# Kernel optimization log

Hardware: AMD Instinct MI355X
Metric: run time of the kernel (lower is better)

## Reference

```python
import jax, jax.numpy as jnp
import numpy as np

CHUNK = 64  # _HYMBA_SCAN_CHUNK default
HEAD_DIM = 128
STATE_DIM = 128


def setup_inputs() -> dict:
    key = jax.random.key(0)
    ks = jax.random.split(key, 6)
    B, T = 8, 8192
    x = jax.random.normal(ks[0], (B, T, HEAD_DIM), dtype=jnp.float32)
    log_A = jax.random.normal(ks[1], (STATE_DIM,), dtype=jnp.float32) * 0.5
    # torch Linear weights are (out_features, in_features); kaiming-uniform-ish init
    lim = 1.0 / np.sqrt(HEAD_DIM)
    W_B = jax.random.uniform(ks[2], (STATE_DIM, HEAD_DIM), jnp.float32, -lim, lim)
    W_C = jax.random.uniform(ks[3], (STATE_DIM, HEAD_DIM), jnp.float32, -lim, lim)
    W_dt = jax.random.uniform(ks[4], (STATE_DIM, HEAD_DIM), jnp.float32, -lim, lim)
    b_dt = jnp.full((STATE_DIM,), -4.0, dtype=jnp.float32)
    lim_o = 1.0 / np.sqrt(STATE_DIM)
    W_out = jax.random.uniform(ks[5], (HEAD_DIM, STATE_DIM), jnp.float32, -lim_o, lim_o)
    return {"x": x, "log_A": log_A, "W_B": W_B, "W_C": W_C,
            "W_dt": W_dt, "b_dt": b_dt, "W_out": W_out}


def _scan_chunks(log_a, u, chunk_size=CHUNK):
    # log_a, u: (B, T, S) fp32; exact chunk-parallel diagonal recurrence
    B, T, S = u.shape
    nc = T // chunk_size
    la = log_a.reshape(B, nc, chunk_size, S).transpose(1, 0, 2, 3)  # (nc,B,ck,S)
    uu = u.reshape(B, nc, chunk_size, S).transpose(1, 0, 2, 3)

    def step(h0, inp):
        la_c, u_c = inp                                   # (B, ck, S)
        log_p = jnp.clip(jnp.cumsum(la_c, axis=1), -30.0, 0.0)
        p = jnp.exp(log_p)
        h = p * jnp.cumsum(u_c * jnp.exp(-log_p), axis=1) + p * h0[:, None, :]
        return h[:, -1, :], h

    h0 = jnp.zeros((B, S), dtype=jnp.float32)
    _, h_chunks = jax.lax.scan(step, h0, (la, uu))        # (nc, B, ck, S)
    return h_chunks.transpose(1, 0, 2, 3).reshape(B, T, S)


def reference(x, log_A, W_B, W_C, W_dt, b_dt, W_out):
    xf = x.astype(jnp.float32)
    dt = jnp.minimum(jax.nn.softplus(jnp.einsum('btd,sd->bts', xf, W_dt) + b_dt), 1.0)
    A = -jnp.minimum(jnp.exp(log_A.astype(jnp.float32)), 10.0)   # (S,)
    log_a = jnp.clip(dt * A[None, None, :], -0.5, 0.0)
    Bx = jnp.einsum('btd,sd->bts', xf, W_B) * dt
    C = jnp.einsum('btd,sd->bts', xf, W_C)
    h = _scan_chunks(log_a, Bx)                                   # (B,T,S)
    y = jnp.sum(C * h, axis=-1, keepdims=True)                    # (B,T,1)
    out = jnp.einsum('bts,ds->btd', h.astype(x.dtype), W_out)
    return out + y.astype(x.dtype) * x[..., :1]
```

## Files before the change

### kernel.cpp

```cpp
#include <hip/hip_runtime.h>
#include <hip/hip_bf16.h>

#define B_ 8
#define T_ 8192
#define D_ 128
#define S_ 128
#define CK 64
#define NC 128
#define NCHUNK (B_*NC)
#define XSTR 140

typedef __attribute__((ext_vector_type(8))) __bf16 bf16x8;
typedef __attribute__((ext_vector_type(4))) float floatx4;

#define WS_WBF     0
#define WS_AVEC    32768
#define WS_PART    32896
#define WS_PARTI   (32896 + 262144)

__device__ __forceinline__ unsigned short f2bf(float f) {
  __hip_bfloat16 b = __float2bfloat16(f);
  return *(unsigned short*)&b;
}

__device__ __forceinline__ float softplus1(float z) {
  float sp = fmaxf(z, 0.0f) + __logf(1.0f + __expf(-fabsf(z)));
  return fminf(sp, 1.0f);
}

__device__ __forceinline__ unsigned long long part_load(const unsigned long long* p) {
  return __hip_atomic_load(p, __ATOMIC_RELAXED, __HIP_MEMORY_SCOPE_AGENT);
}
__device__ __forceinline__ void part_store(unsigned long long* p, unsigned long long v) {
  __hip_atomic_store(p, v, __ATOMIC_RELAXED, __HIP_MEMORY_SCOPE_AGENT);
}

__global__ __launch_bounds__(256) void k0_prep(
    const float* __restrict__ Wdt, const float* __restrict__ WB,
    const float* __restrict__ WC,  const float* __restrict__ Wout,
    const float* __restrict__ logA, float* __restrict__ ws) {
  unsigned short* wb = (unsigned short*)(ws + WS_WBF);
  const float* srcs[4] = {Wdt, WB, WC, Wout};
  int gid = blockIdx.x * 256 + threadIdx.x;
  if (gid < 8192) {
    int fid = gid;
    int lane = fid & 63;
    int kk   = (fid >> 6) & 3;
    int nt   = (fid >> 8) & 7;
    int m    = fid >> 11;
    int c = lane & 15, g = lane >> 4;
    const float* src = srcs[m] + (16 * nt + c) * 128 + 32 * kk + 8 * g;
    float4 v0 = *(const float4*)src;
    float4 v1 = *(const float4*)(src + 4);
    unsigned short o[8];
    o[0] = f2bf(v0.x); o[1] = f2bf(v0.y); o[2] = f2bf(v0.z); o[3] = f2bf(v0.w);
    o[4] = f2bf(v1.x); o[5] = f2bf(v1.y); o[6] = f2bf(v1.z); o[7] = f2bf(v1.w);
    *(ushort4*)&wb[fid * 8]     = *(ushort4*)&o[0];
    *(ushort4*)&wb[fid * 8 + 4] = *(ushort4*)&o[4];
  }
  unsigned long long* part = (unsigned long long*)(ws + WS_PART);
#pragma unroll
  for (int i = 0; i < 16; ++i)
    part[gid + 16384 * i] = 0ull;
  if (blockIdx.x == 0 && threadIdx.x < 128)
    ws[WS_AVEC + threadIdx.x] = -fminf(expf(logA[threadIdx.x]), 10.0f);
}

#define WFRAG(mat, nt, kk) \
  (*(const bf16x8*)&wb[(((((mat) * 8 + (nt)) * 4) + (kk)) * 64 + lane) * 8])

__global__ __launch_bounds__(256, 3) void k_main(
    const float* __restrict__ x, const float* __restrict__ bdt,
    float* __restrict__ out, float* __restrict__ ws) {
  __shared__ __align__(16) unsigned short xb[64 * XSTR];
  __shared__ float x0s[64];
  __shared__ float yxa[4 * 64];

  const int tid  = threadIdx.x;
  const int bc   = blockIdx.x;
  const int b    = bc & 7;
  const int cidx = bc >> 3;
  const long chunk_t0 = (long)b * T_ + (long)cidx * CK;
  const int w    = tid >> 6;
  const int lane = tid & 63;
  const int g    = lane >> 4;
  const int c    = lane & 15;

  float Av2[2], Bd2[2];
#pragma unroll
  for (int ntl = 0; ntl < 2; ++ntl) {
    int s = 32 * w + 16 * ntl + c;
    Av2[ntl] = ws[WS_AVEC + s];
    Bd2[ntl] = bdt[s];
  }

  const float4* x4 = (const float4*)(x + chunk_t0 * D_);
#pragma unroll
  for (int i = 0; i < 8; ++i) {
    int f4 = tid + 256 * i;
    int t  = f4 >> 5;
    int d0 = (f4 & 31) << 2;
    float4 v = x4[f4];
    ushort4 o;
    o.x = f2bf(v.x); o.y = f2bf(v.y); o.z = f2bf(v.z); o.w = f2bf(v.w);
    *(ushort4*)&xb[t * XSTR + d0] = o;
  }
  if (tid < 64) x0s[tid] = x[(chunk_t0 + tid) * D_];
  __syncthreads();

  const unsigned short* wb = (const unsigned short*)(ws + WS_WBF);
  unsigned long long* partA = (unsigned long long*)(ws + WS_PART);
  unsigned long long* partI = (unsigned long long*)(ws + WS_PARTI);

  floatx4 A_[2][4], U_[2][4];
#pragma unroll
  for (int ntl = 0; ntl < 2; ++ntl)
#pragma unroll
    for (int mt = 0; mt < 4; ++mt) {
      A_[ntl][mt] = (floatx4){0.f, 0.f, 0.f, 0.f};
      U_[ntl][mt] = (floatx4){0.f, 0.f, 0.f, 0.f};
    }
#pragma unroll
  for (int kk = 0; kk < 4; ++kk) {
    bf16x8 fD0 = WFRAG(0, 2 * w + 0, kk);
    bf16x8 fD1 = WFRAG(0, 2 * w + 1, kk);
    bf16x8 fB0 = WFRAG(1, 2 * w + 0, kk);
    bf16x8 fB1 = WFRAG(1, 2 * w + 1, kk);
#pragma unroll
    for (int mt = 0; mt < 4; ++mt) {
      bf16x8 a = *(const bf16x8*)&xb[(16 * mt + c) * XSTR + 8 * g + 32 * kk];
      A_[0][mt] = __builtin_amdgcn_mfma_f32_16x16x32_bf16(a, fD0, A_[0][mt], 0, 0, 0);
      A_[1][mt] = __builtin_amdgcn_mfma_f32_16x16x32_bf16(a, fD1, A_[1][mt], 0, 0, 0);
      U_[0][mt] = __builtin_amdgcn_mfma_f32_16x16x32_bf16(a, fB0, U_[0][mt], 0, 0, 0);
      U_[1][mt] = __builtin_amdgcn_mfma_f32_16x16x32_bf16(a, fB1, U_[1][mt], 0, 0, 0);
    }
  }

#pragma unroll
  for (int ntl = 0; ntl < 2; ++ntl)
#pragma unroll
    for (int mt = 0; mt < 4; ++mt)
#pragma unroll
      for (int i = 0; i < 4; ++i) {
        float dt = softplus1(A_[ntl][mt][i] + Bd2[ntl]);
        float u  = U_[ntl][mt][i] * dt;
        float la = fmaxf(fminf(dt * Av2[ntl], 0.0f), -0.5f);
        A_[ntl][mt][i] = __expf(la);
        U_[ntl][mt][i] = u;
      }

  float PcT[2], HcT[2];
#pragma unroll
  for (int ntl = 0; ntl < 2; ++ntl) {
    float Pc = 1.0f, Hc = 0.0f;
#pragma unroll
    for (int mt = 0; mt < 4; ++mt) {
      float P = A_[ntl][mt][0], H = U_[ntl][mt][0];
#pragma unroll
      for (int i = 1; i < 4; ++i) {
        H = fmaf(H, A_[ntl][mt][i], U_[ntl][mt][i]);
        P = P * A_[ntl][mt][i];
        A_[ntl][mt][i] = P;
        U_[ntl][mt][i] = H;
      }
      float Po = __shfl(P, (lane - 16) & 63), Ho = __shfl(H, (lane - 16) & 63);
      if (g >= 1) { H = fmaf(Ho, P, H); P = Po * P; }
      Po = __shfl(P, (lane - 32) & 63); Ho = __shfl(H, (lane - 32) & 63);
      if (g >= 2) { H = fmaf(Ho, P, H); P = Po * P; }
      float Pt = __shfl(P, 48 + c);
      float Ht = __shfl(H, 48 + c);
      float Pe = __shfl(P, (lane - 16) & 63), He = __shfl(H, (lane - 16) & 63);
      if (g == 0) { Pe = 1.0f; He = 0.0f; }
      float Hent = fmaf(Pe, Hc, He);
      float Pent = Pe * Pc;
#pragma unroll
      for (int i = 0; i < 4; ++i) {
        U_[ntl][mt][i] = fmaf(A_[ntl][mt][i], Hent, U_[ntl][mt][i]);
        A_[ntl][mt][i] = A_[ntl][mt][i] * Pent;
      }
      Hc = fmaf(Pt, Hc, Ht);
      Pc = Pc * Pt;
    }
    PcT[ntl] = Pc; HcT[ntl] = Hc;
  }

  if (g == 0) {
#pragma unroll
    for (int ntl = 0; ntl < 2; ++ntl) {
      unsigned long long v = ((unsigned long long)__float_as_uint(HcT[ntl]) << 32) |
                             (unsigned long long)__float_as_uint(PcT[ntl]);
      part_store(&partA[bc * 128 + 32 * w + 16 * ntl + c], v);
    }
  }

  floatx4 Cc[2][4];
#pragma unroll
  for (int ntl = 0; ntl < 2; ++ntl)
#pragma unroll
    for (int mt = 0; mt < 4; ++mt) Cc[ntl][mt] = (floatx4){0.f, 0.f, 0.f, 0.f};
#pragma unroll
  for (int kk = 0; kk < 4; ++kk) {
    bf16x8 fC0 = WFRAG(2, 2 * w + 0, kk);
    bf16x8 fC1 = WFRAG(2, 2 * w + 1, kk);
#pragma unroll
    for (int mt = 0; mt < 4; ++mt) {
      bf16x8 a = *(const bf16x8*)&xb[(16 * mt + c) * XSTR + 8 * g + 32 * kk];
      Cc[0][mt] = __builtin_amdgcn_mfma_f32_16x16x32_bf16(a, fC0, Cc[0][mt], 0, 0, 0);
      Cc[1][mt] = __builtin_amdgcn_mfma_f32_16x16x32_bf16(a, fC1, Cc[1][mt], 0, 0, 0);
    }
  }

  float h0v[2];
  float P0f = 1.0f, H0f = 0.0f;
  {
    const int s = 32 * w + (lane & 31);
    if (lane < 32) {
      float RP = 1.0f, RH = 0.0f;
      int j = cidx - 1;
      while (j >= 0) {
        unsigned long long vi = part_load(&partI[((j << 3) | b) * 128 + s]);
        if ((unsigned)vi != 0u) {
          float Pi = __uint_as_float((unsigned)vi);
          float Hi = __uint_as_float((unsigned)(vi >> 32));
          RH = fmaf(RP, Hi, RH);
          RP = RP * Pi;
          break;
        }
        int nb = (j >= 7) ? 8 : (j + 1);
        unsigned long long v[8];
#pragma unroll
        for (int q = 0; q < 8; ++q)
          if (q < nb) v[q] = part_load(&partA[(((j - q) << 3) | b) * 128 + s]);
#pragma unroll
        for (int q = 0; q < 8; ++q) {
          if (q < nb) {
            unsigned long long vv = v[q];
            const unsigned long long* ap = &partA[(((j - q) << 3) | b) * 128 + s];
            while ((unsigned)vv == 0u) {
              __builtin_amdgcn_s_sleep(2);
              vv = part_load(ap);
            }
            float Pj = __uint_as_float((unsigned)vv);
            float Hj = __uint_as_float((unsigned)(vv >> 32));
            RH = fmaf(RP, Hj, RH);
            RP = RP * Pj;
          }
        }
        j -= nb;
      }
      P0f = RP; H0f = RH;
    }
#pragma unroll
    for (int ntl = 0; ntl < 2; ++ntl)
      h0v[ntl] = __shfl(H0f, 16 * ntl + c);
  }

  if (lane < 32) {
    float Pct = (lane & 16) ? PcT[1] : PcT[0];
    float Hct = (lane & 16) ? HcT[1] : HcT[0];
    float Pinc = fmaxf(Pct * P0f, 1.2e-38f);
    float Hinc = fmaf(Pct, H0f, Hct);
    unsigned long long vI = ((unsigned long long)__float_as_uint(Hinc) << 32) |
                            (unsigned long long)__float_as_uint(Pinc);
    part_store(&partI[bc * 128 + 32 * w + lane], vI);
  }

  __syncthreads();

#pragma unroll
  for (int mt = 0; mt < 4; ++mt) {
    float yv[4] = {0.f, 0.f, 0.f, 0.f};
#pragma unroll
    for (int ntl = 0; ntl < 2; ++ntl)
#pragma unroll
      for (int i = 0; i < 4; ++i) {
        float hv = fmaf(A_[ntl][mt][i], h0v[ntl], U_[ntl][mt][i]);
        yv[i] = fmaf(Cc[ntl][mt][i], hv, yv[i]);
        xb[(16 * mt + 4 * g + i) * XSTR + 32 * w + 16 * ntl + c] = f2bf(hv);
      }
#pragma unroll
    for (int i = 0; i < 4; ++i) {
      float y = yv[i];
      y += __shfl_xor(y, 1);
      y += __shfl_xor(y, 2);
      y += __shfl_xor(y, 4);
      y += __shfl_xor(y, 8);
      if (c == 0) yxa[w * 64 + 16 * mt + 4 * g + i] = y;
    }
  }

  __syncthreads();

  floatx4 Oc[2][4];
#pragma unroll
  for (int ntl = 0; ntl < 2; ++ntl)
#pragma unroll
    for (int mt = 0; mt < 4; ++mt) Oc[ntl][mt] = (floatx4){0.f, 0.f, 0.f, 0.f};
#pragma unroll
  for (int kk = 0; kk < 4; ++kk) {
    bf16x8 fO0 = WFRAG(3, 2 * w + 0, kk);
    bf16x8 fO1 = WFRAG(3, 2 * w + 1, kk);
#pragma unroll
    for (int mt = 0; mt < 4; ++mt) {
      bf16x8 h = *(const bf16x8*)&xb[(16 * mt + c) * XSTR + 8 * g + 32 * kk];
      Oc[0][mt] = __builtin_amdgcn_mfma_f32_16x16x32_bf16(h, fO0, Oc[0][mt], 0, 0, 0);
      Oc[1][mt] = __builtin_amdgcn_mfma_f32_16x16x32_bf16(h, fO1, Oc[1][mt], 0, 0, 0);
    }
  }

#pragma unroll
  for (int mt = 0; mt < 4; ++mt)
#pragma unroll
    for (int i = 0; i < 4; ++i) {
      int row = 16 * mt + 4 * g + i;
      float yt = (yxa[row] + yxa[64 + row] + yxa[128 + row] + yxa[192 + row]) * x0s[row];
#pragma unroll
      for (int ntl = 0; ntl < 2; ++ntl)
        out[(chunk_t0 + row) * D_ + 32 * w + 16 * ntl + c] = Oc[ntl][mt][i] + yt;
    }
}

extern "C" void kernel_launch(void* const* d_in, const int* in_sizes, int n_in,
                              void* d_out, int out_size, void* d_ws, size_t ws_size,
                              hipStream_t stream) {
  const float* x    = (const float*)d_in[0];
  const float* logA = (const float*)d_in[1];
  const float* W_B  = (const float*)d_in[2];
  const float* W_C  = (const float*)d_in[3];
  const float* W_dt = (const float*)d_in[4];
  const float* b_dt = (const float*)d_in[5];
  const float* W_out= (const float*)d_in[6];
  float* out = (float*)d_out;
  float* ws  = (float*)d_ws;

  k0_prep<<<64, 256, 0, stream>>>(W_dt, W_B, W_C, W_out, logA, ws);
  k_main<<<NCHUNK, 256, 0, stream>>>(x, b_dt, out, ws);
}
```

Baseline: 116.5 us.

## Publish first-chunk inclusive prefix early, widen lookback batch, pack bf16 conversions

The first chunk of each sequence now writes its inclusive prefix right after computing the chunk aggregate and skips the lookback entirely. This lets successors find an inclusive value sooner, shortening decoupled-lookback dependency chains. The lookback batch grows from 8 to 16 aggregate loads per iteration, which adds register pressure. Float-to-bf16 conversions use paired conversion intrinsics in the prep kernel, the x staging, and the h writeback.

New measurement: 129.9 us. +11.5%, slower.

```diff
diff --git a/kernel.cpp b/kernel.cpp
--- a/kernel.cpp
+++ b/kernel.cpp
@@ -21,6 +21,11 @@
 __device__ __forceinline__ unsigned short f2bf(float f) {
   __hip_bfloat16 b = __float2bfloat16(f);
   return *(unsigned short*)&b;
+}
+
+__device__ __forceinline__ unsigned int f2bf2(float lo, float hi) {
+  __hip_bfloat162 h2 = __float22bfloat162_rn(make_float2(lo, hi));
+  return *(unsigned int*)&h2;
 }
 
 __device__ __forceinline__ float softplus1(float z) {
@@ -52,11 +57,11 @@
     const float* src = srcs[m] + (16 * nt + c) * 128 + 32 * kk + 8 * g;
     float4 v0 = *(const float4*)src;
     float4 v1 = *(const float4*)(src + 4);
-    unsigned short o[8];
-    o[0] = f2bf(v0.x); o[1] = f2bf(v0.y); o[2] = f2bf(v0.z); o[3] = f2bf(v0.w);
-    o[4] = f2bf(v1.x); o[5] = f2bf(v1.y); o[6] = f2bf(v1.z); o[7] = f2bf(v1.w);
-    *(ushort4*)&wb[fid * 8]     = *(ushort4*)&o[0];
-    *(ushort4*)&wb[fid * 8 + 4] = *(ushort4*)&o[4];
+    unsigned int o[4];
+    o[0] = f2bf2(v0.x, v0.y); o[1] = f2bf2(v0.z, v0.w);
+    o[2] = f2bf2(v1.x, v1.y); o[3] = f2bf2(v1.z, v1.w);
+    *(uint2*)&wb[fid * 8]     = *(uint2*)&o[0];
+    *(uint2*)&wb[fid * 8 + 4] = *(uint2*)&o[2];
   }
   unsigned long long* part = (unsigned long long*)(ws + WS_PART);
 #pragma unroll
@@ -101,9 +106,10 @@
     int t  = f4 >> 5;
     int d0 = (f4 & 31) << 2;
     float4 v = x4[f4];
-    ushort4 o;
-    o.x = f2bf(v.x); o.y = f2bf(v.y); o.z = f2bf(v.z); o.w = f2bf(v.w);
-    *(ushort4*)&xb[t * XSTR + d0] = o;
+    unsigned int o[2];
+    o[0] = f2bf2(v.x, v.y);
+    o[1] = f2bf2(v.z, v.w);
+    *(uint2*)&xb[t * XSTR + d0] = *(uint2*)&o[0];
   }
   if (tid < 64) x0s[tid] = x[(chunk_t0 + tid) * D_];
   __syncthreads();
@@ -192,6 +198,13 @@
       part_store(&partA[bc * 128 + 32 * w + 16 * ntl + c], v);
     }
   }
+  if (cidx == 0 && lane < 32) {
+    float Pct = (lane & 16) ? PcT[1] : PcT[0];
+    float Hct = (lane & 16) ? HcT[1] : HcT[0];
+    unsigned long long vI = ((unsigned long long)__float_as_uint(Hct) << 32) |
+                            (unsigned long long)__float_as_uint(fmaxf(Pct, 1.2e-38f));
+    part_store(&partI[bc * 128 + 32 * w + lane], vI);
+  }
 
   floatx4 Cc[2][4];
 #pragma unroll
@@ -214,7 +227,7 @@
   float P0f = 1.0f, H0f = 0.0f;
   {
     const int s = 32 * w + (lane & 31);
-    if (lane < 32) {
+    if (lane < 32 && cidx > 0) {
       float RP = 1.0f, RH = 0.0f;
       int j = cidx - 1;
       while (j >= 0) {
@@ -226,13 +239,13 @@
           RP = RP * Pi;
           break;
         }
-        int nb = (j >= 7) ? 8 : (j + 1);
-        unsigned long long v[8];
-#pragma unroll
-        for (int q = 0; q < 8; ++q)
+        int nb = (j >= 15) ? 16 : (j + 1);
+        unsigned long long v[16];
+#pragma unroll
+        for (int q = 0; q < 16; ++q)
           if (q < nb) v[q] = part_load(&partA[(((j - q) << 3) | b) * 128 + s]);
 #pragma unroll
-        for (int q = 0; q < 8; ++q) {
+        for (int q = 0; q < 16; ++q) {
           if (q < nb) {
             unsigned long long vv = v[q];
             const unsigned long long* ap = &partA[(((j - q) << 3) | b) * 128 + s];
@@ -255,7 +268,7 @@
       h0v[ntl] = __shfl(H0f, 16 * ntl + c);
   }
 
-  if (lane < 32) {
+  if (lane < 32 && cidx > 0) {
     float Pct = (lane & 16) ? PcT[1] : PcT[0];
     float Hct = (lane & 16) ? HcT[1] : HcT[0];
     float Pinc = fmaxf(Pct * P0f, 1.2e-38f);
@@ -271,13 +284,16 @@
   for (int mt = 0; mt < 4; ++mt) {
     float yv[4] = {0.f, 0.f, 0.f, 0.f};
 #pragma unroll
-    for (int ntl = 0; ntl < 2; ++ntl)
-#pragma unroll
-      for (int i = 0; i < 4; ++i) {
-        float hv = fmaf(A_[ntl][mt][i], h0v[ntl], U_[ntl][mt][i]);
-        yv[i] = fmaf(Cc[ntl][mt][i], hv, yv[i]);
-        xb[(16 * mt + 4 * g + i) * XSTR + 32 * w + 16 * ntl + c] = f2bf(hv);
-      }
+    for (int i = 0; i < 4; ++i) {
+      float hv0 = fmaf(A_[0][mt][i], h0v[0], U_[0][mt][i]);
+      float hv1 = fmaf(A_[1][mt][i], h0v[1], U_[1][mt][i]);
+      yv[i] = fmaf(Cc[0][mt][i], hv0, yv[i]);
+      yv[i] = fmaf(Cc[1][mt][i], hv1, yv[i]);
+      unsigned int hp = f2bf2(hv0, hv1);
+      int rb = (16 * mt + 4 * g + i) * XSTR + 32 * w + c;
+      xb[rb]      = (unsigned short)hp;
+      xb[rb + 16] = (unsigned short)(hp >> 16);
+    }
 #pragma unroll
     for (int i = 0; i < 4; ++i) {
       float y = yv[i];
```

## Split each chunk block across 8 waves with one state tile per wave

Applied to the files above, without the earlier changes.

Grows the main kernel block from 256 to 512 threads so each wave owns a single 16-wide state tile rather than two. This halves per-thread registers and MFMA chains and spreads the serial scan and decoupled-lookback work over more waves. It also lets chunk 0 publish its inclusive prefix right away and skip the lookback, which shortens the dependency chain for later chunks. The cost is larger block-wide syncs and an 8-way y reduction through shared memory, and occupancy now depends on the 512,6 launch bound being met.

New measurement: 132.9 us. 1.14x slower.

```diff
diff --git a/kernel.cpp b/kernel.cpp
--- a/kernel.cpp
+++ b/kernel.cpp
@@ -69,12 +69,12 @@
 #define WFRAG(mat, nt, kk) \
   (*(const bf16x8*)&wb[(((((mat) * 8 + (nt)) * 4) + (kk)) * 64 + lane) * 8])
 
-__global__ __launch_bounds__(256, 3) void k_main(
+__global__ __launch_bounds__(512, 6) void k_main(
     const float* __restrict__ x, const float* __restrict__ bdt,
     float* __restrict__ out, float* __restrict__ ws) {
   __shared__ __align__(16) unsigned short xb[64 * XSTR];
   __shared__ float x0s[64];
-  __shared__ float yxa[4 * 64];
+  __shared__ float yxa[8 * 64];
 
   const int tid  = threadIdx.x;
   const int bc   = blockIdx.x;
@@ -86,18 +86,13 @@
   const int g    = lane >> 4;
   const int c    = lane & 15;
 
-  float Av2[2], Bd2[2];
-#pragma unroll
-  for (int ntl = 0; ntl < 2; ++ntl) {
-    int s = 32 * w + 16 * ntl + c;
-    Av2[ntl] = ws[WS_AVEC + s];
-    Bd2[ntl] = bdt[s];
-  }
+  const float Av = ws[WS_AVEC + 16 * w + c];
+  const float Bd = bdt[16 * w + c];
 
   const float4* x4 = (const float4*)(x + chunk_t0 * D_);
 #pragma unroll
-  for (int i = 0; i < 8; ++i) {
-    int f4 = tid + 256 * i;
+  for (int i = 0; i < 4; ++i) {
+    int f4 = tid + 512 * i;
     int t  = f4 >> 5;
     int d0 = (f4 & 31) << 2;
     float4 v = x4[f4];
@@ -112,56 +107,47 @@
   unsigned long long* partA = (unsigned long long*)(ws + WS_PART);
   unsigned long long* partI = (unsigned long long*)(ws + WS_PARTI);
 
-  floatx4 A_[2][4], U_[2][4];
-#pragma unroll
-  for (int ntl = 0; ntl < 2; ++ntl)
-#pragma unroll
-    for (int mt = 0; mt < 4; ++mt) {
-      A_[ntl][mt] = (floatx4){0.f, 0.f, 0.f, 0.f};
-      U_[ntl][mt] = (floatx4){0.f, 0.f, 0.f, 0.f};
-    }
+  floatx4 A_[4], U_[4];
+#pragma unroll
+  for (int mt = 0; mt < 4; ++mt) {
+    A_[mt] = (floatx4){0.f, 0.f, 0.f, 0.f};
+    U_[mt] = (floatx4){0.f, 0.f, 0.f, 0.f};
+  }
 #pragma unroll
   for (int kk = 0; kk < 4; ++kk) {
-    bf16x8 fD0 = WFRAG(0, 2 * w + 0, kk);
-    bf16x8 fD1 = WFRAG(0, 2 * w + 1, kk);
-    bf16x8 fB0 = WFRAG(1, 2 * w + 0, kk);
-    bf16x8 fB1 = WFRAG(1, 2 * w + 1, kk);
+    bf16x8 fD = WFRAG(0, w, kk);
+    bf16x8 fB = WFRAG(1, w, kk);
 #pragma unroll
     for (int mt = 0; mt < 4; ++mt) {
       bf16x8 a = *(const bf16x8*)&xb[(16 * mt + c) * XSTR + 8 * g + 32 * kk];
-      A_[0][mt] = __builtin_amdgcn_mfma_f32_16x16x32_bf16(a, fD0, A_[0][mt], 0, 0, 0);
-      A_[1][mt] = __builtin_amdgcn_mfma_f32_16x16x32_bf16(a, fD1, A_[1][mt], 0, 0, 0);
-      U_[0][mt] = __builtin_amdgcn_mfma_f32_16x16x32_bf16(a, fB0, U_[0][mt], 0, 0, 0);
-      U_[1][mt] = __builtin_amdgcn_mfma_f32_16x16x32_bf16(a, fB1, U_[1][mt], 0, 0, 0);
-    }
-  }
-
-#pragma unroll
-  for (int ntl = 0; ntl < 2; ++ntl)
-#pragma unroll
-    for (int mt = 0; mt < 4; ++mt)
-#pragma unroll
-      for (int i = 0; i < 4; ++i) {
-        float dt = softplus1(A_[ntl][mt][i] + Bd2[ntl]);
-        float u  = U_[ntl][mt][i] * dt;
-        float la = fmaxf(fminf(dt * Av2[ntl], 0.0f), -0.5f);
-        A_[ntl][mt][i] = __expf(la);
-        U_[ntl][mt][i] = u;
-      }
-
-  float PcT[2], HcT[2];
-#pragma unroll
-  for (int ntl = 0; ntl < 2; ++ntl) {
+      A_[mt] = __builtin_amdgcn_mfma_f32_16x16x32_bf16(a, fD, A_[mt], 0, 0, 0);
+      U_[mt] = __builtin_amdgcn_mfma_f32_16x16x32_bf16(a, fB, U_[mt], 0, 0, 0);
+    }
+  }
+
+#pragma unroll
+  for (int mt = 0; mt < 4; ++mt)
+#pragma unroll
+    for (int i = 0; i < 4; ++i) {
+      float dt = softplus1(A_[mt][i] + Bd);
+      float u  = U_[mt][i] * dt;
+      float la = fmaxf(fminf(dt * Av, 0.0f), -0.5f);
+      A_[mt][i] = __expf(la);
+      U_[mt][i] = u;
+    }
+
+  float PcT, HcT;
+  {
     float Pc = 1.0f, Hc = 0.0f;
 #pragma unroll
     for (int mt = 0; mt < 4; ++mt) {
-      float P = A_[ntl][mt][0], H = U_[ntl][mt][0];
+      float P = A_[mt][0], H = U_[mt][0];
 #pragma unroll
       for (int i = 1; i < 4; ++i) {
-        H = fmaf(H, A_[ntl][mt][i], U_[ntl][mt][i]);
-        P = P * A_[ntl][mt][i];
-        A_[ntl][mt][i] = P;
-        U_[ntl][mt][i] = H;
+        H = fmaf(H, A_[mt][i], U_[mt][i]);
+        P = P * A_[mt][i];
+        A_[mt][i] = P;
+        U_[mt][i] = H;
       }
       float Po = __shfl(P, (lane - 16) & 63), Ho = __shfl(H, (lane - 16) & 63);
       if (g >= 1) { H = fmaf(Ho, P, H); P = Po * P; }
@@ -175,46 +161,44 @@
       float Pent = Pe * Pc;
 #pragma unroll
       for (int i = 0; i < 4; ++i) {
-        U_[ntl][mt][i] = fmaf(A_[ntl][mt][i], Hent, U_[ntl][mt][i]);
-        A_[ntl][mt][i] = A_[ntl][mt][i] * Pent;
+        U_[mt][i] = fmaf(A_[mt][i], Hent, U_[mt][i]);
+        A_[mt][i] = A_[mt][i] * Pent;
       }
       Hc = fmaf(Pt, Hc, Ht);
       Pc = Pc * Pt;
     }
-    PcT[ntl] = Pc; HcT[ntl] = Hc;
+    PcT = Pc; HcT = Hc;
   }
 
   if (g == 0) {
-#pragma unroll
-    for (int ntl = 0; ntl < 2; ++ntl) {
-      unsigned long long v = ((unsigned long long)__float_as_uint(HcT[ntl]) << 32) |
-                             (unsigned long long)__float_as_uint(PcT[ntl]);
-      part_store(&partA[bc * 128 + 32 * w + 16 * ntl + c], v);
-    }
-  }
-
-  floatx4 Cc[2][4];
-#pragma unroll
-  for (int ntl = 0; ntl < 2; ++ntl)
-#pragma unroll
-    for (int mt = 0; mt < 4; ++mt) Cc[ntl][mt] = (floatx4){0.f, 0.f, 0.f, 0.f};
+    unsigned long long v = ((unsigned long long)__float_as_uint(HcT) << 32) |
+                           (unsigned long long)__float_as_uint(PcT);
+    part_store(&partA[bc * 128 + 16 * w + c], v);
+  }
+  if (cidx == 0 && lane < 16) {
+    unsigned long long vI = ((unsigned long long)__float_as_uint(HcT) << 32) |
+                            (unsigned long long)__float_as_uint(fmaxf(PcT, 1.2e-38f));
+    part_store(&partI[bc * 128 + 16 * w + lane], vI);
+  }
+
+  floatx4 Cc[4];
+#pragma unroll
+  for (int mt = 0; mt < 4; ++mt) Cc[mt] = (floatx4){0.f, 0.f, 0.f, 0.f};
 #pragma unroll
   for (int kk = 0; kk < 4; ++kk) {
-    bf16x8 fC0 = WFRAG(2, 2 * w + 0, kk);
-    bf16x8 fC1 = WFRAG(2, 2 * w + 1, kk);
+    bf16x8 fC = WFRAG(2, w, kk);
 #pragma unroll
     for (int mt = 0; mt < 4; ++mt) {
       bf16x8 a = *(const bf16x8*)&xb[(16 * mt + c) * XSTR + 8 * g + 32 * kk];
-      Cc[0][mt] = __builtin_amdgcn_mfma_f32_16x16x32_bf16(a, fC0, Cc[0][mt], 0, 0, 0);
-      Cc[1][mt] = __builtin_amdgcn_mfma_f32_16x16x32_bf16(a, fC1, Cc[1][mt], 0, 0, 0);
-    }
-  }
-
-  float h0v[2];
-  float P0f = 1.0f, H0f = 0.0f;
+      Cc[mt] = __builtin_amdgcn_mfma_f32_16x16x32_bf16(a, fC, Cc[mt], 0, 0, 0);
+    }
+  }
+
+  float h0;
   {
-    const int s = 32 * w + (lane & 31);
-    if (lane < 32) {
+    float P0f = 1.0f, H0f = 0.0f;
+    const int s = 16 * w + (lane & 15);
+    if (lane < 16 && cidx > 0) {
       float RP = 1.0f, RH = 0.0f;
       int j = cidx - 1;
       while (j >= 0) {
@@ -250,34 +234,27 @@
       }
       P0f = RP; H0f = RH;
     }
-#pragma unroll
-    for (int ntl = 0; ntl < 2; ++ntl)
-      h0v[ntl] = __shfl(H0f, 16 * ntl + c);
-  }
-
-  if (lane < 32) {
-    float Pct = (lane & 16) ? PcT[1] : PcT[0];
-    float Hct = (lane & 16) ? HcT[1] : HcT[0];
-    float Pinc = fmaxf(Pct * P0f, 1.2e-38f);
-    float Hinc = fmaf(Pct, H0f, Hct);
-    unsigned long long vI = ((unsigned long long)__float_as_uint(Hinc) << 32) |
-                            (unsigned long long)__float_as_uint(Pinc);
-    part_store(&partI[bc * 128 + 32 * w + lane], vI);
+    if (lane < 16 && cidx > 0) {
+      float Pinc = fmaxf(PcT * P0f, 1.2e-38f);
+      float Hinc = fmaf(PcT, H0f, HcT);
+      unsigned long long vI = ((unsigned long long)__float_as_uint(Hinc) << 32) |
+                              (unsigned long long)__float_as_uint(Pinc);
+      part_store(&partI[bc * 128 + 16 * w + lane], vI);
+    }
+    h0 = __shfl(H0f, c);
   }
 
   __syncthreads();
 
 #pragma unroll
   for (int mt = 0; mt < 4; ++mt) {
-    float yv[4] = {0.f, 0.f, 0.f, 0.f};
-#pragma unroll
-    for (int ntl = 0; ntl < 2; ++ntl)
-#pragma unroll
-      for (int i = 0; i < 4; ++i) {
-        float hv = fmaf(A_[ntl][mt][i], h0v[ntl], U_[ntl][mt][i]);
-        yv[i] = fmaf(Cc[ntl][mt][i], hv, yv[i]);
-        xb[(16 * mt + 4 * g + i) * XSTR + 32 * w + 16 * ntl + c] = f2bf(hv);
-      }
+    float yv[4];
+#pragma unroll
+    for (int i = 0; i < 4; ++i) {
+      float hv = fmaf(A_[mt][i], h0, U_[mt][i]);
+      yv[i] = Cc[mt][i] * hv;
+      xb[(16 * mt + 4 * g + i) * XSTR + 16 * w + c] = f2bf(hv);
+    }
 #pragma unroll
     for (int i = 0; i < 4; ++i) {
       float y = yv[i];
@@ -291,20 +268,16 @@
 
   __syncthreads();
 
-  floatx4 Oc[2][4];
-#pragma unroll
-  for (int ntl = 0; ntl < 2; ++ntl)
-#pragma unroll
-    for (int mt = 0; mt < 4; ++mt) Oc[ntl][mt] = (floatx4){0.f, 0.f, 0.f, 0.f};
+  floatx4 Oc[4];
+#pragma unroll
+  for (int mt = 0; mt < 4; ++mt) Oc[mt] = (floatx4){0.f, 0.f, 0.f, 0.f};
 #pragma unroll
   for (int kk = 0; kk < 4; ++kk) {
-    bf16x8 fO0 = WFRAG(3, 2 * w + 0, kk);
-    bf16x8 fO1 = WFRAG(3, 2 * w + 1, kk);
+    bf16x8 fO = WFRAG(3, w, kk);
 #pragma unroll
     for (int mt = 0; mt < 4; ++mt) {
       bf16x8 h = *(const bf16x8*)&xb[(16 * mt + c) * XSTR + 8 * g + 32 * kk];
-      Oc[0][mt] = __builtin_amdgcn_mfma_f32_16x16x32_bf16(h, fO0, Oc[0][mt], 0, 0, 0);
-      Oc[1][mt] = __builtin_amdgcn_mfma_f32_16x16x32_bf16(h, fO1, Oc[1][mt], 0, 0, 0);
+      Oc[mt] = __builtin_amdgcn_mfma_f32_16x16x32_bf16(h, fO, Oc[mt], 0, 0, 0);
     }
   }
 
@@ -313,10 +286,11 @@
 #pragma unroll
     for (int i = 0; i < 4; ++i) {
       int row = 16 * mt + 4 * g + i;
-      float yt = (yxa[row] + yxa[64 + row] + yxa[128 + row] + yxa[192 + row]) * x0s[row];
-#pragma unroll
-      for (int ntl = 0; ntl < 2; ++ntl)
-        out[(chunk_t0 + row) * D_ + 32 * w + 16 * ntl + c] = Oc[ntl][mt][i] + yt;
+      float yt = 0.0f;
+#pragma unroll
+      for (int ww = 0; ww < 8; ++ww) yt += yxa[ww * 64 + row];
+      yt *= x0s[row];
+      out[(chunk_t0 + row) * D_ + 16 * w + c] = Oc[mt][i] + yt;
     }
 }
 
@@ -334,5 +308,5 @@
   float* ws  = (float*)d_ws;
 
   k0_prep<<<64, 256, 0, stream>>>(W_dt, W_B, W_C, W_out, logA, ws);
-  k_main<<<NCHUNK, 256, 0, stream>>>(x, b_dt, out, ws);
-}
+  k_main<<<NCHUNK, 512, 0, stream>>>(x, b_dt, out, ws);
+}
```
